# Kernel optimization log

Measured on AMD Instinct MI355X. Metric: run time of the kernel, lower is better.

Reference implementation:

```python
import jax, jax.numpy as jnp
import numpy as np

EPSILON = 1e-05
LOG_2PI = float(np.log(2.0 * np.pi))


def setup_inputs() -> dict:
    key = jax.random.key(0)
    k1, k2, k3 = jax.random.split(key, 3)
    B, S, K, N = 64, 1000, 12, 80  # batch, seq, n_states, n_channels
    x = jax.random.normal(k1, (B, S, N), dtype=jnp.float32)
    mu = jax.random.normal(k2, (B, K, N), dtype=jnp.float32)
    # Positive-definite covariances per (batch, state)
    A = jax.random.normal(k3, (B, K, N, N), dtype=jnp.float32)
    sigma = A @ jnp.swapaxes(A, -1, -2) / N + jnp.eye(N, dtype=jnp.float32)
    return {"x": x, "mu": mu, "sigma": sigma}


def reference(x, mu, sigma):
    """Batched-over-states MVN log-likelihood.

    x: (B, S, N); mu: (B, K, N); sigma: (B, K, N, N).
    Returns log_likelihood: (B, S, K).
    """
    N = x.shape[-1]
    # add_epsilon with diag=True: epsilon * I on the diagonal
    sigma = sigma + jnp.asarray(EPSILON, sigma.dtype) * jnp.eye(N, dtype=sigma.dtype)
    L = jnp.linalg.cholesky(sigma)  # (B, K, N, N), batched across states
    diff = x[:, :, None, :] - mu[:, None, :, :]  # (B, S, K, N)
    # Solve L z = diff, batched: L -> (B, 1, K, N, N), diff -> (B, S, K, N, 1)
    z = jax.scipy.linalg.solve_triangular(L[:, None], diff[..., None], lower=True)[..., 0]
    quad = jnp.sum(z * z, axis=-1)  # (B, S, K)
    logdet_half = jnp.sum(jnp.log(jnp.diagonal(L, axis1=-2, axis2=-1)), axis=-1)  # (B, K)
    ll = -0.5 * quad - logdet_half[:, None, :] - 0.5 * N * jnp.asarray(LOG_2PI, x.dtype)
    return ll  # (B, S, K)
```

## Files before the change

### kernel.cpp

```cpp
#include <hip/hip_runtime.h>

#define Bb 64
#define Ss 1000
#define Kk 12
#define Nn 80
#define CTERM 73.51508265637381f
#define STA 84

typedef __attribute__((ext_vector_type(8))) short short8;
typedef __attribute__((ext_vector_type(4))) float f32x4;

static __device__ __forceinline__ unsigned short f2bf(float f) {
    unsigned u = __builtin_bit_cast(unsigned, f);
    unsigned r = u + 0x7FFFu + ((u >> 16) & 1u);
    return (unsigned short)(r >> 16);
}
static __device__ __forceinline__ float bf2f(unsigned short h) {
    unsigned u = ((unsigned)h) << 16;
    return __builtin_bit_cast(float, u);
}

__global__ __launch_bounds__(512, 6) void prep_kernel(
    const float* __restrict__ sigma, const float* __restrict__ mu,
    const float* __restrict__ x,
    uint4* __restrict__ wsWh, uint4* __restrict__ wsWl,
    float* __restrict__ wsV, float* __restrict__ wsL,
    uint4* __restrict__ Xh, uint4* __restrict__ Xl, int doX)
{
    __shared__ float Ls[Nn * STA];
    __shared__ float invd[Nn];
    __shared__ float mus[Nn];
    __shared__ float ldp[8];
    __shared__ float vps[8 * Nn];

    const int bk  = blockIdx.x;
    const int tid = threadIdx.x;
    const int w   = tid >> 6;
    const int l   = tid & 63;
    const int r2  = l + 64;

    const float4* sp4 = (const float4*)(sigma + (size_t)bk * Nn * Nn);
    #pragma unroll
    for (int it = 0; it < 4; ++it) {
        int ci = tid + 512 * it;
        if (ci < 1600) {
            int r = ci / 20, c4 = 4 * (ci - 20 * r);
            if (c4 <= r + 3) {
                float4 v = sp4[ci];
                *(float4*)&Ls[r * STA + c4] = v;
            }
        }
    }
    if (tid < Nn) mus[tid] = mu[(size_t)bk * Nn + tid];
    __syncthreads();
    if (tid < Nn) Ls[tid * STA + tid] += 1e-5f;
    __syncthreads();

    float ldacc = 0.0f;
    for (int p = 0; p < 20; ++p) {
        const int j0 = 4 * p;
        const bool a1 = (l >= j0);
        const bool a2 = (l < 16) && (r2 >= j0);

        if (w == (p & 7)) {
            float B00 = Ls[j0*STA+j0];
            float B10 = Ls[(j0+1)*STA+j0], B11 = Ls[(j0+1)*STA+j0+1];
            float B20 = Ls[(j0+2)*STA+j0], B21 = Ls[(j0+2)*STA+j0+1], B22 = Ls[(j0+2)*STA+j0+2];
            float B30 = Ls[(j0+3)*STA+j0], B31 = Ls[(j0+3)*STA+j0+1], B32 = Ls[(j0+3)*STA+j0+2], B33 = Ls[(j0+3)*STA+j0+3];
            float rv0 = rsqrtf(B00);
            float l10 = B10*rv0, l20 = B20*rv0, l30 = B30*rv0;
            float t11 = fmaf(-l10,l10,B11);                    float rv1 = rsqrtf(t11);
            float l21 = fmaf(-l20,l10,B21)*rv1;
            float l31 = fmaf(-l30,l10,B31)*rv1;
            float t22 = fmaf(-l21,l21,fmaf(-l20,l20,B22));     float rv2 = rsqrtf(t22);
            float l32 = fmaf(-l31,l21,fmaf(-l30,l20,B32))*rv2;
            float t33 = fmaf(-l32,l32,fmaf(-l31,l31,fmaf(-l30,l30,B33)));
            float rv3 = rsqrtf(t33);
            ldacc += 0.5f * (logf(B00) + logf(t11) + logf(t22) + logf(t33));
            if (l == 0) { invd[j0]=rv0; invd[j0+1]=rv1; invd[j0+2]=rv2; invd[j0+3]=rv3; }

            if (a1) {
                float4 a = *(float4*)&Ls[l * STA + j0];
                float b0 = a.x * rv0;
                float b1 = fmaf(-l10, b0, a.y) * rv1;
                float b2 = fmaf(-l21, b1, fmaf(-l20, b0, a.z)) * rv2;
                float b3 = fmaf(-l32, b2, fmaf(-l31, b1, fmaf(-l30, b0, a.w))) * rv3;
                *(float4*)&Ls[l * STA + j0] = make_float4(b0, b1, b2, b3);
            }
            if (a2) {
                float4 a = *(float4*)&Ls[r2 * STA + j0];
                float c0 = a.x * rv0;
                float c1 = fmaf(-l10, c0, a.y) * rv1;
                float c2 = fmaf(-l21, c1, fmaf(-l20, c0, a.z)) * rv2;
                float c3 = fmaf(-l32, c2, fmaf(-l31, c1, fmaf(-l30, c0, a.w))) * rv3;
                *(float4*)&Ls[r2 * STA + j0] = make_float4(c0, c1, c2, c3);
            }
        }
        __syncthreads();

        const int gs0 = p + 1;
        const int g0 = gs0 + ((w - gs0) & 7);
        #pragma unroll 2
        for (int g = g0; g < 20; g += 8) {
            const int cb = 4 * g;
            float4 q0 = *(const float4*)&Ls[(cb+0) * STA + j0];
            float4 q1 = *(const float4*)&Ls[(cb+1) * STA + j0];
            float4 q2 = *(const float4*)&Ls[(cb+2) * STA + j0];
            float4 q3 = *(const float4*)&Ls[(cb+3) * STA + j0];
            {
                const int R = cb + l;
                if (R < Nn) {
                    float4 pv = *(const float4*)&Ls[R * STA + j0];
                    float4 t  = *(float4*)&Ls[R * STA + cb];
                    t.x = fmaf(-pv.x,q0.x, fmaf(-pv.y,q0.y, fmaf(-pv.z,q0.z, fmaf(-pv.w,q0.w, t.x))));
                    t.y = fmaf(-pv.x,q1.x, fmaf(-pv.y,q1.y, fmaf(-pv.z,q1.z, fmaf(-pv.w,q1.w, t.y))));
                    t.z = fmaf(-pv.x,q2.x, fmaf(-pv.y,q2.y, fmaf(-pv.z,q2.z, fmaf(-pv.w,q2.w, t.z))));
                    t.w = fmaf(-pv.x,q3.x, fmaf(-pv.y,q3.y, fmaf(-pv.z,q3.z, fmaf(-pv.w,q3.w, t.w))));
                    *(float4*)&Ls[R * STA + cb] = t;
                }
            }
            if (cb + 64 < Nn) {
                const int R = cb + 64 + l;
                if (R < Nn) {
                    float4 pv = *(const float4*)&Ls[R * STA + j0];
                    float4 t  = *(float4*)&Ls[R * STA + cb];
                    t.x = fmaf(-pv.x,q0.x, fmaf(-pv.y,q0.y, fmaf(-pv.z,q0.z, fmaf(-pv.w,q0.w, t.x))));
                    t.y = fmaf(-pv.x,q1.x, fmaf(-pv.y,q1.y, fmaf(-pv.z,q1.z, fmaf(-pv.w,q1.w, t.y))));
                    t.z = fmaf(-pv.x,q2.x, fmaf(-pv.y,q2.y, fmaf(-pv.z,q2.z, fmaf(-pv.w,q2.w, t.z))));
                    t.w = fmaf(-pv.x,q3.x, fmaf(-pv.y,q3.y, fmaf(-pv.z,q3.z, fmaf(-pv.w,q3.w, t.w))));
                    *(float4*)&Ls[R * STA + cb] = t;
                }
            }
        }
    }
    if (l == 0) ldp[w] = ldacc;
    __syncthreads();
    if (tid == 0) wsL[bk] = ldp[0]+ldp[1]+ldp[2]+ldp[3]+ldp[4]+ldp[5]+ldp[6]+ldp[7];

    for (int i = tid; i < Nn * Nn; i += 512) {
        int r = i / Nn, c = i - Nn * r;
        if (c > r) Ls[r * STA + c] = 0.0f;
    }
    __syncthreads();

    for (int p = 0; p < 20; ++p) {
        const int i0 = 4 * p;
        const bool b1a = (i0 + 3 >= l);
        const bool b2a = (l < 16) && (i0 + 3 >= r2);

        if (w == (p & 7)) {
            float m10 = Ls[(i0+1)*STA + i0];
            float m20 = Ls[(i0+2)*STA + i0];
            float m30 = Ls[(i0+3)*STA + i0];
            float m21 = Ls[(i0+2)*STA + i0+1];
            float m31 = Ls[(i0+3)*STA + i0+1];
            float m32 = Ls[(i0+3)*STA + i0+2];
            float4 iv = *(const float4*)&invd[i0];
            if (b1a) {
                float4 a = *(float4*)&Ls[l * STA + i0];
                if (l >= i0)
                    a = make_float4(l==i0?1.f:0.f, l==i0+1?1.f:0.f, l==i0+2?1.f:0.f, l==i0+3?1.f:0.f);
                float w0 = a.x * iv.x;
                float w1 = fmaf(-w0, m10, a.y) * iv.y;
                float w2 = fmaf(-w1, m21, fmaf(-w0, m20, a.z)) * iv.z;
                float w3 = fmaf(-w2, m32, fmaf(-w1, m31, fmaf(-w0, m30, a.w))) * iv.w;
                *(float4*)&Ls[l * STA + i0] = make_float4(w0, w1, w2, w3);
            }
            if (b2a) {
                float4 a = *(float4*)&Ls[r2 * STA + i0];
                if (r2 >= i0)
                    a = make_float4(r2==i0?1.f:0.f, r2==i0+1?1.f:0.f, r2==i0+2?1.f:0.f, r2==i0+3?1.f:0.f);
                float v0 = a.x * iv.x;
                float v1 = fmaf(-v0, m10, a.y) * iv.y;
                float v2 = fmaf(-v1, m21, fmaf(-v0, m20, a.z)) * iv.z;
                float v3 = fmaf(-v2, m32, fmaf(-v1, m31, fmaf(-v0, m30, a.w))) * iv.w;
                *(float4*)&Ls[r2 * STA + i0] = make_float4(v0, v1, v2, v3);
            }
        }
        __syncthreads();

        float4 wv = make_float4(0.f,0.f,0.f,0.f), vv = make_float4(0.f,0.f,0.f,0.f);
        if (b1a) wv = *(float4*)&Ls[l * STA + i0];
        if (b2a) vv = *(float4*)&Ls[r2 * STA + i0];
        if (b1a | b2a) {
            const int gs0 = p + 1;
            const int g0 = gs0 + ((w - gs0) & 7);
            for (int g = g0; g < 20; g += 8) {
                float4 q0 = *(const float4*)&Ls[(4*g+0) * STA + i0];
                float4 q1 = *(const float4*)&Ls[(4*g+1) * STA + i0];
                float4 q2 = *(const float4*)&Ls[(4*g+2) * STA + i0];
                float4 q3 = *(const float4*)&Ls[(4*g+3) * STA + i0];
                if (b1a) {
                    float4 t = *(float4*)&Ls[l * STA + 4*g];
                    t.x = fmaf(-wv.x,q0.x, fmaf(-wv.y,q0.y, fmaf(-wv.z,q0.z, fmaf(-wv.w,q0.w, t.x))));
                    t.y = fmaf(-wv.x,q1.x, fmaf(-wv.y,q1.y, fmaf(-wv.z,q1.z, fmaf(-wv.w,q1.w, t.y))));
                    t.z = fmaf(-wv.x,q2.x, fmaf(-wv.y,q2.y, fmaf(-wv.z,q2.z, fmaf(-wv.w,q2.w, t.z))));
                    t.w = fmaf(-wv.x,q3.x, fmaf(-wv.y,q3.y, fmaf(-wv.z,q3.z, fmaf(-wv.w,q3.w, t.w))));
                    *(float4*)&Ls[l * STA + 4*g] = t;
                }
                if (b2a) {
                    float4 t = *(float4*)&Ls[r2 * STA + 4*g];
                    t.x = fmaf(-vv.x,q0.x, fmaf(-vv.y,q0.y, fmaf(-vv.z,q0.z, fmaf(-vv.w,q0.w, t.x))));
                    t.y = fmaf(-vv.x,q1.x, fmaf(-vv.y,q1.y, fmaf(-vv.z,q1.z, fmaf(-vv.w,q1.w, t.y))));
                    t.z = fmaf(-vv.x,q2.x, fmaf(-vv.y,q2.y, fmaf(-vv.z,q2.z, fmaf(-vv.w,q2.w, t.z))));
                    t.w = fmaf(-vv.x,q3.x, fmaf(-vv.y,q3.y, fmaf(-vv.z,q3.z, fmaf(-vv.w,q3.w, t.w))));
                    *(float4*)&Ls[r2 * STA + 4*g] = t;
                }
            }
        }
    }
    __syncthreads();

    {
        float s1 = 0.f, s2 = 0.f;
        const int c0 = 10 * w;
        #pragma unroll 2
        for (int cc = 0; cc < 10; ++cc) {
            int c = c0 + cc;
            float mc = mus[c];
            float e1 = (c <= l)  ? Ls[c * STA + l]  : 0.f;
            s1 = fmaf(e1, mc, s1);
            if (l < 16) {
                float e2 = (c <= r2) ? Ls[c * STA + r2] : 0.f;
                s2 = fmaf(e2, mc, s2);
            }
        }
        vps[w * Nn + l] = s1;
        if (l < 16) vps[w * Nn + r2] = s2;
        __syncthreads();
        if (tid < Nn) {
            float acc = 0.f;
            #pragma unroll
            for (int ww = 0; ww < 8; ++ww) acc += vps[ww * Nn + tid];
            wsV[(size_t)bk * Nn + tid] = acc;
        }
    }

    const int n = l & 15, quad = l >> 4;
    uint4* ph = wsWh + (size_t)bk * 800;
    uint4* pq = wsWl + (size_t)bk * 800;
    for (int f = w; f < 10; f += 8) {
        int ks = f / 5, mt = f - 5 * ks;
        int m = 16 * mt + n, kb = 32 * ks + 8 * quad;
        unsigned hh[8], lo[8];
        #pragma unroll
        for (int j = 0; j < 8; ++j) {
            float wj = (m >= kb + j) ? Ls[(kb + j) * STA + m] : 0.f;
            unsigned short h = f2bf(wj);
            hh[j] = h; lo[j] = f2bf(wj - bf2f(h));
        }
        ph[f*64 + l] = make_uint4(hh[0]|(hh[1]<<16), hh[2]|(hh[3]<<16), hh[4]|(hh[5]<<16), hh[6]|(hh[7]<<16));
        pq[f*64 + l] = make_uint4(lo[0]|(lo[1]<<16), lo[2]|(lo[3]<<16), lo[4]|(lo[5]<<16), lo[6]|(lo[7]<<16));
    }
    if (w < 5) {
        int mt = w;
        if (quad < 2) {
            int m = 16 * mt + n, kb = 64 + 8 * quad;
            unsigned hh[8], lo[8];
            #pragma unroll
            for (int j = 0; j < 8; ++j) {
                float wj = (m >= kb + j) ? Ls[(kb + j) * STA + m] : 0.f;
                unsigned short h = f2bf(wj);
                hh[j] = h; lo[j] = f2bf(wj - bf2f(h));
            }
            ph[640 + mt*32 + l] = make_uint4(hh[0]|(hh[1]<<16), hh[2]|(hh[3]<<16), hh[4]|(hh[5]<<16), hh[6]|(hh[7]<<16));
            pq[640 + mt*32 + l] = make_uint4(lo[0]|(lo[1]<<16), lo[2]|(lo[3]<<16), lo[4]|(lo[5]<<16), lo[6]|(lo[7]<<16));
        }
    }

    if (doX) {
        const int wid = bk * 8 + w;
        const int qd = l >> 4, n2 = l & 15;
        #pragma unroll
        for (int it = 0; it < 2; ++it) {
            int G = wid + 6144 * it;
            if (G >= 12096) break;
            int b2  = G / 189;
            int rem = G - b2 * 189;
            int sg  = rem / 3, ks = rem - 3 * sg;
            int s   = sg * 16 + n2;
            int k0  = 32 * ks + 8 * qd;
            float d[8] = {0.f,0.f,0.f,0.f,0.f,0.f,0.f,0.f};
            if (s < Ss) {
                const float* xp = x + ((size_t)b2 * Ss + s) * Nn + k0;
                float4 f0 = *(const float4*)xp;
                float4 f1 = *(const float4*)(xp + 4);
                d[0]=f0.x; d[1]=f0.y; d[2]=f0.z; d[3]=f0.w;
                d[4]=f1.x; d[5]=f1.y; d[6]=f1.z; d[7]=f1.w;
            }
            unsigned hh[8], lo[8];
            #pragma unroll
            for (int j = 0; j < 8; ++j) {
                unsigned short h = f2bf(d[j]);
                hh[j] = h; lo[j] = f2bf(d[j] - bf2f(h));
            }
            size_t slot = ((size_t)(b2 * 64 + sg) * 3 + ks) * 64 + l;
            Xh[slot] = make_uint4(hh[0]|(hh[1]<<16), hh[2]|(hh[3]<<16), hh[4]|(hh[5]<<16), hh[6]|(hh[7]<<16));
            Xl[slot] = make_uint4(lo[0]|(lo[1]<<16), lo[2]|(lo[3]<<16), lo[4]|(lo[5]<<16), lo[6]|(lo[7]<<16));
        }
    }
}

__global__ __launch_bounds__(256) void ll_kernel2(
    const uint4* __restrict__ Xh, const uint4* __restrict__ Xl,
    const uint4* __restrict__ wsWh, const uint4* __restrict__ wsWl,
    const float* __restrict__ wsV, const float* __restrict__ wsL,
    float* __restrict__ out)
{
    __shared__ uint4 WhL[960], WlL[960];
    const int b = blockIdx.x;
    const int k = blockIdx.y;
    const int bk = b * Kk + k;
    const int tid = threadIdx.x;
    const int wv = tid >> 6, lane = tid & 63;
    const int n = lane & 15, quad = lane >> 4;

    const uint4* gh = wsWh + (size_t)bk * 800;
    const uint4* gl = wsWl + (size_t)bk * 800;
    #pragma unroll
    for (int it = 0; it < 3; ++it) {
        int i = tid + 256 * it;
        if (i < 640) { WhL[i] = gh[i]; WlL[i] = gl[i]; }
    }
    #pragma unroll
    for (int it = 0; it < 2; ++it) {
        int i = tid + 256 * it;
        if (i < 320) {
            int mt = i >> 6, ln = i & 63, qd = (ln >> 4);
            uint4 vh = make_uint4(0,0,0,0), vl = make_uint4(0,0,0,0);
            if (qd < 2) { vh = gh[640 + mt*32 + ln]; vl = gl[640 + mt*32 + ln]; }
            WhL[640 + i] = vh; WlL[640 + i] = vl;
        }
    }
    __syncthreads();

    const float ld = wsL[bk];
    f32x4 vf[5];
    #pragma unroll
    for (int mt = 0; mt < 5; ++mt)
        vf[mt] = *(const f32x4*)&wsV[(size_t)bk * Nn + 16*mt + 4*quad];

    for (int st = 0; st < 8; ++st) {
        const int sg0 = st * 8 + wv * 2;
        short8 bh[2][3], bl[2][3];
        #pragma unroll
        for (int t = 0; t < 2; ++t)
            #pragma unroll
            for (int ks = 0; ks < 3; ++ks) {
                size_t base = ((size_t)(b * 64 + sg0 + t) * 3 + ks) * 64 + lane;
                bh[t][ks] = __builtin_bit_cast(short8, Xh[base]);
                bl[t][ks] = __builtin_bit_cast(short8, Xl[base]);
            }

        f32x4 acc[2][5];
        #pragma unroll
        for (int t = 0; t < 2; ++t)
            #pragma unroll
            for (int mt = 0; mt < 5; ++mt) acc[t][mt] = (f32x4){0.f,0.f,0.f,0.f};

        #pragma unroll
        for (int ks = 0; ks < 3; ++ks) {
            #pragma unroll
            for (int mt = 0; mt < 5; ++mt) {
                const int fi = (ks < 2) ? (ks*5 + mt)*64 + lane : 640 + mt*64 + lane;
                short8 wh = __builtin_bit_cast(short8, WhL[fi]);
                short8 wl = __builtin_bit_cast(short8, WlL[fi]);
                #pragma unroll
                for (int t = 0; t < 2; ++t) {
                    acc[t][mt] = __builtin_amdgcn_mfma_f32_16x16x32_bf16(wh, bh[t][ks], acc[t][mt], 0, 0, 0);
                    acc[t][mt] = __builtin_amdgcn_mfma_f32_16x16x32_bf16(wl, bh[t][ks], acc[t][mt], 0, 0, 0);
                    acc[t][mt] = __builtin_amdgcn_mfma_f32_16x16x32_bf16(wh, bl[t][ks], acc[t][mt], 0, 0, 0);
                }
            }
        }

        #pragma unroll
        for (int t = 0; t < 2; ++t) {
            float q2 = 0.f;
            #pragma unroll
            for (int mt = 0; mt < 5; ++mt)
                #pragma unroll
                for (int r = 0; r < 4; ++r) {
                    float y = acc[t][mt][r] - vf[mt][r];
                    q2 = fmaf(y, y, q2);
                }
            q2 += __shfl_xor(q2, 16, 64);
            q2 += __shfl_xor(q2, 32, 64);
            int gs = st * 128 + wv * 32 + 16 * t + n;
            if (lane < 16 && gs < Ss)
                out[((size_t)b * Ss + gs) * Kk + k] = -0.5f * q2 - ld - CTERM;
        }
    }
}

__global__ __launch_bounds__(256) void ll_kernel(
    const float* __restrict__ x,
    const uint4* __restrict__ wsWh, const uint4* __restrict__ wsWl,
    const float* __restrict__ wsV, const float* __restrict__ wsL,
    float* __restrict__ out)
{
    const int b    = blockIdx.x;
    const int st   = blockIdx.y;
    const int tid  = threadIdx.x;
    const int wv   = tid >> 6, lane = tid & 63;
    const int n    = lane & 15, quad = lane >> 4;
    const int sbase = st * 128 + wv * 32;

    short8 xh[2][3], xl[2][3];
    #pragma unroll
    for (int t = 0; t < 2; ++t) {
        int gs = sbase + 16 * t + n;
        #pragma unroll
        for (int ks = 0; ks < 3; ++ks) {
            int kb = 32 * ks + 8 * quad;
            float d[8] = {0.f,0.f,0.f,0.f,0.f,0.f,0.f,0.f};
            if (gs < Ss && kb < Nn) {
                const float* xp = x + ((size_t)b * Ss + gs) * Nn + kb;
                float4 f0 = *(const float4*)xp;
                float4 f1 = *(const float4*)(xp + 4);
                d[0]=f0.x; d[1]=f0.y; d[2]=f0.z; d[3]=f0.w;
                d[4]=f1.x; d[5]=f1.y; d[6]=f1.z; d[7]=f1.w;
            }
            short8 h, lo2;
            #pragma unroll
            for (int j = 0; j < 8; ++j) {
                unsigned short hv = f2bf(d[j]);
                h[j]   = (short)hv;
                lo2[j] = (short)f2bf(d[j] - bf2f(hv));
            }
            xh[t][ks] = h; xl[t][ks] = lo2;
        }
    }

    for (int k = 0; k < Kk; ++k) {
        const int bk = b * Kk + k;
        const uint4* ah_p = wsWh + (size_t)bk * 800;
        const uint4* al_p = wsWl + (size_t)bk * 800;

        f32x4 acc[2][5];
        #pragma unroll
        for (int t = 0; t < 2; ++t)
            #pragma unroll
            for (int mt = 0; mt < 5; ++mt) acc[t][mt] = (f32x4){0.f,0.f,0.f,0.f};

        #pragma unroll
        for (int ks = 0; ks < 3; ++ks) {
            short8 ah[5], al[5];
            if (ks < 2) {
                #pragma unroll
                for (int mt = 0; mt < 5; ++mt) {
                    ah[mt] = __builtin_bit_cast(short8, ah_p[(ks*5 + mt)*64 + lane]);
                    al[mt] = __builtin_bit_cast(short8, al_p[(ks*5 + mt)*64 + lane]);
                }
            } else {
                #pragma unroll
                for (int mt = 0; mt < 5; ++mt) {
                    uint4 zh = make_uint4(0,0,0,0), zl = make_uint4(0,0,0,0);
                    if (quad < 2) {
                        zh = ah_p[640 + mt*32 + lane];
                        zl = al_p[640 + mt*32 + lane];
                    }
                    ah[mt] = __builtin_bit_cast(short8, zh);
                    al[mt] = __builtin_bit_cast(short8, zl);
                }
            }
            #pragma unroll
            for (int mt = 0; mt < 5; ++mt)
                #pragma unroll
                for (int t = 0; t < 2; ++t) {
                    acc[t][mt] = __builtin_amdgcn_mfma_f32_16x16x32_bf16(ah[mt], xh[t][ks], acc[t][mt], 0, 0, 0);
                    acc[t][mt] = __builtin_amdgcn_mfma_f32_16x16x32_bf16(al[mt], xh[t][ks], acc[t][mt], 0, 0, 0);
                    acc[t][mt] = __builtin_amdgcn_mfma_f32_16x16x32_bf16(ah[mt], xl[t][ks], acc[t][mt], 0, 0, 0);
                }
        }

        float ld = wsL[bk];
        f32x4 vf[5];
        #pragma unroll
        for (int mt = 0; mt < 5; ++mt)
            vf[mt] = *(const f32x4*)&wsV[(size_t)bk * Nn + 16*mt + 4*quad];
        #pragma unroll
        for (int t = 0; t < 2; ++t) {
            float q2 = 0.f;
            #pragma unroll
            for (int mt = 0; mt < 5; ++mt)
                #pragma unroll
                for (int r = 0; r < 4; ++r) {
                    float y = acc[t][mt][r] - vf[mt][r];
                    q2 = fmaf(y, y, q2);
                }
            q2 += __shfl_xor(q2, 16, 64);
            q2 += __shfl_xor(q2, 32, 64);
            int gs = sbase + 16 * t + n;
            if (lane < 16 && gs < Ss)
                out[((size_t)b * Ss + gs) * Kk + k] = -0.5f * q2 - ld - CTERM;
        }
    }
}

#define ST1 81
__global__ __launch_bounds__(256) void mvn_ll_fallback(
    const float* __restrict__ x, const float* __restrict__ mu,
    const float* __restrict__ sigma, float* __restrict__ out)
{
    __shared__ float Ls[Nn * ST1];
    __shared__ float invd[Nn];
    __shared__ float mus[Nn];
    __shared__ float logdet_s;

    const int bk = blockIdx.x, b = bk / Kk, k = bk - b * Kk;
    const int tid = threadIdx.x, nt = blockDim.x;

    const float* sp = sigma + (size_t)bk * Nn * Nn;
    for (int t = tid; t < Nn * Nn; t += nt) Ls[(t / Nn) * ST1 + (t % Nn)] = sp[t];
    if (tid < Nn) mus[tid] = mu[(size_t)bk * Nn + tid];
    __syncthreads();
    if (tid < Nn) Ls[tid * ST1 + tid] += 1e-5f;
    __syncthreads();
    for (int j = 0; j < Nn; ++j) {
        if (tid == 0) {
            float d = sqrtf(Ls[j * ST1 + j]);
            Ls[j * ST1 + j] = d; invd[j] = 1.0f / d;
        }
        __syncthreads();
        const float inv = invd[j];
        for (int i = j + 1 + tid; i < Nn; i += nt) Ls[i * ST1 + j] *= inv;
        __syncthreads();
        for (int t = tid; t < Nn * Nn; t += nt) {
            int r = t / Nn, c = t % Nn;
            if (r > j && c > j && c <= r)
                Ls[r * ST1 + c] -= Ls[r * ST1 + j] * Ls[c * ST1 + j];
        }
        __syncthreads();
    }
    if (tid == 0) {
        float a = 0.f; for (int j = 0; j < Nn; ++j) a += logf(Ls[j * ST1 + j]);
        logdet_s = a;
    }
    __syncthreads();
    const float ld = logdet_s;
    for (int s = tid; s < Ss; s += nt) {
        const float4* xp = (const float4*)(x + ((size_t)b * Ss + s) * Nn);
        float a[Nn];
        #pragma unroll
        for (int q = 0; q < Nn / 4; ++q) {
            float4 v = xp[q];
            a[4*q+0] = v.x - mus[4*q+0]; a[4*q+1] = v.y - mus[4*q+1];
            a[4*q+2] = v.z - mus[4*q+2]; a[4*q+3] = v.w - mus[4*q+3];
        }
        #pragma unroll
        for (int i = 0; i < Nn; ++i) {
            float t = a[i];
            #pragma unroll
            for (int j = 0; j < i; ++j) t = fmaf(-Ls[i * ST1 + j], a[j], t);
            a[i] = t * invd[i];
        }
        float quad = 0.f;
        #pragma unroll
        for (int i = 0; i < Nn; ++i) quad = fmaf(a[i], a[i], quad);
        out[((size_t)b * Ss + s) * Kk + k] = -0.5f * quad - ld - CTERM;
    }
}

extern "C" void kernel_launch(void* const* d_in, const int* in_sizes, int n_in,
                              void* d_out, int out_size, void* d_ws, size_t ws_size,
                              hipStream_t stream) {
    const float* x     = (const float*)d_in[0];
    const float* mu    = (const float*)d_in[1];
    const float* sigma = (const float*)d_in[2];
    float* out = (float*)d_out;

    const size_t nBK   = (size_t)Bb * Kk;
    const size_t nWu4  = nBK * 800;
    const size_t nXu4  = (size_t)Bb * 64 * 3 * 64;
    const size_t need_mid  = nWu4 * 16 * 2 + nBK * Nn * 4 + nBK * 4;
    const size_t need_full = need_mid + nXu4 * 16 * 2;

    if (ws_size >= need_full) {
        uint4* wsWh = (uint4*)d_ws;
        uint4* wsWl = wsWh + nWu4;
        uint4* Xh   = wsWl + nWu4;
        uint4* Xl   = Xh + nXu4;
        float* wsV  = (float*)(Xl + nXu4);
        float* wsL  = wsV + nBK * Nn;
        prep_kernel<<<dim3(Bb * Kk), dim3(512), 0, stream>>>(
            sigma, mu, x, wsWh, wsWl, wsV, wsL, Xh, Xl, 1);
        ll_kernel2<<<dim3(Bb, Kk), dim3(256), 0, stream>>>(Xh, Xl, wsWh, wsWl, wsV, wsL, out);
    } else if (ws_size >= need_mid) {
        uint4* wsWh = (uint4*)d_ws;
        uint4* wsWl = wsWh + nWu4;
        float* wsV  = (float*)(wsWl + nWu4);
        float* wsL  = wsV + nBK * Nn;
        prep_kernel<<<dim3(Bb * Kk), dim3(512), 0, stream>>>(
            sigma, mu, x, wsWh, wsWl, wsV, wsL, (uint4*)nullptr, (uint4*)nullptr, 0);
        ll_kernel<<<dim3(Bb, 8), dim3(256), 0, stream>>>(x, wsWh, wsWl, wsV, wsL, out);
    } else {
        mvn_ll_fallback<<<dim3(Bb * Kk), dim3(256), 0, stream>>>(x, mu, sigma, out);
    }
}
```

Before: 161.6 us.

## Run Cholesky and inverse in a single wave, overlapping X conversion on second wave

The prep kernel shrinks from 512 to 128 threads. Wave 0 now does the whole Cholesky factorisation, triangular inverse and mu projection alone, with no block barriers. Wave 1 meanwhile converts x into split-bf16 tiles, and both waves then pack the W fragments. This removes roughly 40 __syncthreads per block and the shared-memory reductions, and also switches to fast __logf. The cost is serialising the factorisation into one wave, so per-block latency grows while more blocks can be resident per CU.

Result: slower. 209.5 us (+29.6%).

```diff
diff --git a/kernel.cpp b/kernel.cpp
--- a/kernel.cpp
+++ b/kernel.cpp
@@ -20,7 +20,7 @@
     return __builtin_bit_cast(float, u);
 }
 
-__global__ __launch_bounds__(512, 6) void prep_kernel(
+__global__ __launch_bounds__(128, 2) void prep_kernel(
     const float* __restrict__ sigma, const float* __restrict__ mu,
     const float* __restrict__ x,
     uint4* __restrict__ wsWh, uint4* __restrict__ wsWl,
@@ -30,8 +30,6 @@
     __shared__ float Ls[Nn * STA];
     __shared__ float invd[Nn];
     __shared__ float mus[Nn];
-    __shared__ float ldp[8];
-    __shared__ float vps[8 * Nn];
 
     const int bk  = blockIdx.x;
     const int tid = threadIdx.x;
@@ -39,30 +37,23 @@
     const int l   = tid & 63;
     const int r2  = l + 64;
 
-    const float4* sp4 = (const float4*)(sigma + (size_t)bk * Nn * Nn);
-    #pragma unroll
-    for (int it = 0; it < 4; ++it) {
-        int ci = tid + 512 * it;
-        if (ci < 1600) {
+    if (w == 0) {
+        const float4* sp4 = (const float4*)(sigma + (size_t)bk * Nn * Nn);
+        #pragma unroll
+        for (int it = 0; it < 25; ++it) {
+            int ci = l + 64 * it;
             int r = ci / 20, c4 = 4 * (ci - 20 * r);
-            if (c4 <= r + 3) {
-                float4 v = sp4[ci];
-                *(float4*)&Ls[r * STA + c4] = v;
-            }
-        }
-    }
-    if (tid < Nn) mus[tid] = mu[(size_t)bk * Nn + tid];
-    __syncthreads();
-    if (tid < Nn) Ls[tid * STA + tid] += 1e-5f;
-    __syncthreads();
-
-    float ldacc = 0.0f;
-    for (int p = 0; p < 20; ++p) {
-        const int j0 = 4 * p;
-        const bool a1 = (l >= j0);
-        const bool a2 = (l < 16) && (r2 >= j0);
-
-        if (w == (p & 7)) {
+            if (c4 <= r + 3)
+                *(float4*)&Ls[r * STA + c4] = sp4[ci];
+        }
+        mus[l] = mu[(size_t)bk * Nn + l];
+        if (l < 16) mus[r2] = mu[(size_t)bk * Nn + r2];
+        Ls[l * STA + l] += 1e-5f;
+        if (l < 16) Ls[r2 * STA + r2] += 1e-5f;
+
+        float ldacc = 0.0f;
+        for (int p = 0; p < 20; ++p) {
+            const int j0 = 4 * p;
             float B00 = Ls[j0*STA+j0];
             float B10 = Ls[(j0+1)*STA+j0], B11 = Ls[(j0+1)*STA+j0+1];
             float B20 = Ls[(j0+2)*STA+j0], B21 = Ls[(j0+2)*STA+j0+1], B22 = Ls[(j0+2)*STA+j0+2];
@@ -76,10 +67,10 @@
             float l32 = fmaf(-l31,l21,fmaf(-l30,l20,B32))*rv2;
             float t33 = fmaf(-l32,l32,fmaf(-l31,l31,fmaf(-l30,l30,B33)));
             float rv3 = rsqrtf(t33);
-            ldacc += 0.5f * (logf(B00) + logf(t11) + logf(t22) + logf(t33));
+            ldacc += 0.5f * (__logf(B00) + __logf(t11) + __logf(t22) + __logf(t33));
             if (l == 0) { invd[j0]=rv0; invd[j0+1]=rv1; invd[j0+2]=rv2; invd[j0+3]=rv3; }
 
-            if (a1) {
+            if (l >= j0) {
                 float4 a = *(float4*)&Ls[l * STA + j0];
                 float b0 = a.x * rv0;
                 float b1 = fmaf(-l10, b0, a.y) * rv1;
@@ -87,7 +78,7 @@
                 float b3 = fmaf(-l32, b2, fmaf(-l31, b1, fmaf(-l30, b0, a.w))) * rv3;
                 *(float4*)&Ls[l * STA + j0] = make_float4(b0, b1, b2, b3);
             }
-            if (a2) {
+            if (l < 16 && r2 >= j0) {
                 float4 a = *(float4*)&Ls[r2 * STA + j0];
                 float c0 = a.x * rv0;
                 float c1 = fmaf(-l10, c0, a.y) * rv1;
@@ -95,60 +86,47 @@
                 float c3 = fmaf(-l32, c2, fmaf(-l31, c1, fmaf(-l30, c0, a.w))) * rv3;
                 *(float4*)&Ls[r2 * STA + j0] = make_float4(c0, c1, c2, c3);
             }
-        }
-        __syncthreads();
-
-        const int gs0 = p + 1;
-        const int g0 = gs0 + ((w - gs0) & 7);
-        #pragma unroll 2
-        for (int g = g0; g < 20; g += 8) {
-            const int cb = 4 * g;
-            float4 q0 = *(const float4*)&Ls[(cb+0) * STA + j0];
-            float4 q1 = *(const float4*)&Ls[(cb+1) * STA + j0];
-            float4 q2 = *(const float4*)&Ls[(cb+2) * STA + j0];
-            float4 q3 = *(const float4*)&Ls[(cb+3) * STA + j0];
-            {
-                const int R = cb + l;
-                if (R < Nn) {
-                    float4 pv = *(const float4*)&Ls[R * STA + j0];
-                    float4 t  = *(float4*)&Ls[R * STA + cb];
-                    t.x = fmaf(-pv.x,q0.x, fmaf(-pv.y,q0.y, fmaf(-pv.z,q0.z, fmaf(-pv.w,q0.w, t.x))));
-                    t.y = fmaf(-pv.x,q1.x, fmaf(-pv.y,q1.y, fmaf(-pv.z,q1.z, fmaf(-pv.w,q1.w, t.y))));
-                    t.z = fmaf(-pv.x,q2.x, fmaf(-pv.y,q2.y, fmaf(-pv.z,q2.z, fmaf(-pv.w,q2.w, t.z))));
-                    t.w = fmaf(-pv.x,q3.x, fmaf(-pv.y,q3.y, fmaf(-pv.z,q3.z, fmaf(-pv.w,q3.w, t.w))));
-                    *(float4*)&Ls[R * STA + cb] = t;
-                }
-            }
-            if (cb + 64 < Nn) {
-                const int R = cb + 64 + l;
-                if (R < Nn) {
-                    float4 pv = *(const float4*)&Ls[R * STA + j0];
-                    float4 t  = *(float4*)&Ls[R * STA + cb];
-                    t.x = fmaf(-pv.x,q0.x, fmaf(-pv.y,q0.y, fmaf(-pv.z,q0.z, fmaf(-pv.w,q0.w, t.x))));
-                    t.y = fmaf(-pv.x,q1.x, fmaf(-pv.y,q1.y, fmaf(-pv.z,q1.z, fmaf(-pv.w,q1.w, t.y))));
-                    t.z = fmaf(-pv.x,q2.x, fmaf(-pv.y,q2.y, fmaf(-pv.z,q2.z, fmaf(-pv.w,q2.w, t.z))));
-                    t.w = fmaf(-pv.x,q3.x, fmaf(-pv.y,q3.y, fmaf(-pv.z,q3.z, fmaf(-pv.w,q3.w, t.w))));
-                    *(float4*)&Ls[R * STA + cb] = t;
-                }
-            }
-        }
-    }
-    if (l == 0) ldp[w] = ldacc;
-    __syncthreads();
-    if (tid == 0) wsL[bk] = ldp[0]+ldp[1]+ldp[2]+ldp[3]+ldp[4]+ldp[5]+ldp[6]+ldp[7];
-
-    for (int i = tid; i < Nn * Nn; i += 512) {
-        int r = i / Nn, c = i - Nn * r;
-        if (c > r) Ls[r * STA + c] = 0.0f;
-    }
-    __syncthreads();
-
-    for (int p = 0; p < 20; ++p) {
-        const int i0 = 4 * p;
-        const bool b1a = (i0 + 3 >= l);
-        const bool b2a = (l < 16) && (i0 + 3 >= r2);
-
-        if (w == (p & 7)) {
+
+            #pragma unroll 2
+            for (int g = p + 1; g < 20; ++g) {
+                const int cb = 4 * g;
+                float4 q0 = *(const float4*)&Ls[(cb+0) * STA + j0];
+                float4 q1 = *(const float4*)&Ls[(cb+1) * STA + j0];
+                float4 q2 = *(const float4*)&Ls[(cb+2) * STA + j0];
+                float4 q3 = *(const float4*)&Ls[(cb+3) * STA + j0];
+                {
+                    const int R = cb + l;
+                    if (R < Nn) {
+                        float4 pv = *(const float4*)&Ls[R * STA + j0];
+                        float4 t  = *(float4*)&Ls[R * STA + cb];
+                        t.x = fmaf(-pv.x,q0.x, fmaf(-pv.y,q0.y, fmaf(-pv.z,q0.z, fmaf(-pv.w,q0.w, t.x))));
+                        t.y = fmaf(-pv.x,q1.x, fmaf(-pv.y,q1.y, fmaf(-pv.z,q1.z, fmaf(-pv.w,q1.w, t.y))));
+                        t.z = fmaf(-pv.x,q2.x, fmaf(-pv.y,q2.y, fmaf(-pv.z,q2.z, fmaf(-pv.w,q2.w, t.z))));
+                        t.w = fmaf(-pv.x,q3.x, fmaf(-pv.y,q3.y, fmaf(-pv.z,q3.z, fmaf(-pv.w,q3.w, t.w))));
+                        *(float4*)&Ls[R * STA + cb] = t;
+                    }
+                }
+                if (cb + 64 < Nn) {
+                    const int R = cb + 64 + l;
+                    if (R < Nn) {
+                        float4 pv = *(const float4*)&Ls[R * STA + j0];
+                        float4 t  = *(float4*)&Ls[R * STA + cb];
+                        t.x = fmaf(-pv.x,q0.x, fmaf(-pv.y,q0.y, fmaf(-pv.z,q0.z, fmaf(-pv.w,q0.w, t.x))));
+                        t.y = fmaf(-pv.x,q1.x, fmaf(-pv.y,q1.y, fmaf(-pv.z,q1.z, fmaf(-pv.w,q1.w, t.y))));
+                        t.z = fmaf(-pv.x,q2.x, fmaf(-pv.y,q2.y, fmaf(-pv.z,q2.z, fmaf(-pv.w,q2.w, t.z))));
+                        t.w = fmaf(-pv.x,q3.x, fmaf(-pv.y,q3.y, fmaf(-pv.z,q3.z, fmaf(-pv.w,q3.w, t.w))));
+                        *(float4*)&Ls[R * STA + cb] = t;
+                    }
+                }
+            }
+        }
+        if (l == 0) wsL[bk] = ldacc;
+
+        for (int p = 0; p < 20; ++p) {
+            const int i0 = 4 * p;
+            const bool b1a = (i0 + 3 >= l);
+            const bool b2a = (l < 16) && (i0 + 3 >= r2);
+
             float m10 = Ls[(i0+1)*STA + i0];
             float m20 = Ls[(i0+2)*STA + i0];
             float m30 = Ls[(i0+3)*STA + i0];
@@ -156,124 +134,85 @@
             float m31 = Ls[(i0+3)*STA + i0+1];
             float m32 = Ls[(i0+3)*STA + i0+2];
             float4 iv = *(const float4*)&invd[i0];
+
+            float sw0=0.f, sw1=0.f, sw2=0.f, sw3=0.f;
+            float sv0=0.f, sv1=0.f, sv2=0.f, sv3=0.f;
             if (b1a) {
-                float4 a = *(float4*)&Ls[l * STA + i0];
+                float4 a;
                 if (l >= i0)
                     a = make_float4(l==i0?1.f:0.f, l==i0+1?1.f:0.f, l==i0+2?1.f:0.f, l==i0+3?1.f:0.f);
-                float w0 = a.x * iv.x;
-                float w1 = fmaf(-w0, m10, a.y) * iv.y;
-                float w2 = fmaf(-w1, m21, fmaf(-w0, m20, a.z)) * iv.z;
-                float w3 = fmaf(-w2, m32, fmaf(-w1, m31, fmaf(-w0, m30, a.w))) * iv.w;
-                *(float4*)&Ls[l * STA + i0] = make_float4(w0, w1, w2, w3);
+                else
+                    a = *(float4*)&Ls[l * STA + i0];
+                sw0 = a.x * iv.x;
+                sw1 = fmaf(-sw0, m10, a.y) * iv.y;
+                sw2 = fmaf(-sw1, m21, fmaf(-sw0, m20, a.z)) * iv.z;
+                sw3 = fmaf(-sw2, m32, fmaf(-sw1, m31, fmaf(-sw0, m30, a.w))) * iv.w;
+                *(float4*)&Ls[l * STA + i0] = make_float4(sw0, sw1, sw2, sw3);
             }
             if (b2a) {
-                float4 a = *(float4*)&Ls[r2 * STA + i0];
+                float4 a;
                 if (r2 >= i0)
                     a = make_float4(r2==i0?1.f:0.f, r2==i0+1?1.f:0.f, r2==i0+2?1.f:0.f, r2==i0+3?1.f:0.f);
-                float v0 = a.x * iv.x;
-                float v1 = fmaf(-v0, m10, a.y) * iv.y;
-                float v2 = fmaf(-v1, m21, fmaf(-v0, m20, a.z)) * iv.z;
-                float v3 = fmaf(-v2, m32, fmaf(-v1, m31, fmaf(-v0, m30, a.w))) * iv.w;
-                *(float4*)&Ls[r2 * STA + i0] = make_float4(v0, v1, v2, v3);
-            }
-        }
-        __syncthreads();
-
-        float4 wv = make_float4(0.f,0.f,0.f,0.f), vv = make_float4(0.f,0.f,0.f,0.f);
-        if (b1a) wv = *(float4*)&Ls[l * STA + i0];
-        if (b2a) vv = *(float4*)&Ls[r2 * STA + i0];
-        if (b1a | b2a) {
-            const int gs0 = p + 1;
-            const int g0 = gs0 + ((w - gs0) & 7);
-            for (int g = g0; g < 20; g += 8) {
-                float4 q0 = *(const float4*)&Ls[(4*g+0) * STA + i0];
-                float4 q1 = *(const float4*)&Ls[(4*g+1) * STA + i0];
-                float4 q2 = *(const float4*)&Ls[(4*g+2) * STA + i0];
-                float4 q3 = *(const float4*)&Ls[(4*g+3) * STA + i0];
-                if (b1a) {
-                    float4 t = *(float4*)&Ls[l * STA + 4*g];
-                    t.x = fmaf(-wv.x,q0.x, fmaf(-wv.y,q0.y, fmaf(-wv.z,q0.z, fmaf(-wv.w,q0.w, t.x))));
-                    t.y = fmaf(-wv.x,q1.x, fmaf(-wv.y,q1.y, fmaf(-wv.z,q1.z, fmaf(-wv.w,q1.w, t.y))));
-                    t.z = fmaf(-wv.x,q2.x, fmaf(-wv.y,q2.y, fmaf(-wv.z,q2.z, fmaf(-wv.w,q2.w, t.z))));
-                    t.w = fmaf(-wv.x,q3.x, fmaf(-wv.y,q3.y, fmaf(-wv.z,q3.z, fmaf(-wv.w,q3.w, t.w))));
-                    *(float4*)&Ls[l * STA + 4*g] = t;
-                }
-                if (b2a) {
-                    float4 t = *(float4*)&Ls[r2 * STA + 4*g];
-                    t.x = fmaf(-vv.x,q0.x, fmaf(-vv.y,q0.y, fmaf(-vv.z,q0.z, fmaf(-vv.w,q0.w, t.x))));
-                    t.y = fmaf(-vv.x,q1.x, fmaf(-vv.y,q1.y, fmaf(-vv.z,q1.z, fmaf(-vv.w,q1.w, t.y))));
-                    t.z = fmaf(-vv.x,q2.x, fmaf(-vv.y,q2.y, fmaf(-vv.z,q2.z, fmaf(-vv.w,q2.w, t.z))));
-                    t.w = fmaf(-vv.x,q3.x, fmaf(-vv.y,q3.y, fmaf(-vv.z,q3.z, fmaf(-vv.w,q3.w, t.w))));
-                    *(float4*)&Ls[r2 * STA + 4*g] = t;
-                }
-            }
-        }
-    }
-    __syncthreads();
-
-    {
-        float s1 = 0.f, s2 = 0.f;
-        const int c0 = 10 * w;
-        #pragma unroll 2
-        for (int cc = 0; cc < 10; ++cc) {
-            int c = c0 + cc;
-            float mc = mus[c];
-            float e1 = (c <= l)  ? Ls[c * STA + l]  : 0.f;
-            s1 = fmaf(e1, mc, s1);
-            if (l < 16) {
-                float e2 = (c <= r2) ? Ls[c * STA + r2] : 0.f;
-                s2 = fmaf(e2, mc, s2);
-            }
-        }
-        vps[w * Nn + l] = s1;
-        if (l < 16) vps[w * Nn + r2] = s2;
-        __syncthreads();
-        if (tid < Nn) {
-            float acc = 0.f;
-            #pragma unroll
-            for (int ww = 0; ww < 8; ++ww) acc += vps[ww * Nn + tid];
-            wsV[(size_t)bk * Nn + tid] = acc;
-        }
-    }
-
-    const int n = l & 15, quad = l >> 4;
-    uint4* ph = wsWh + (size_t)bk * 800;
-    uint4* pq = wsWl + (size_t)bk * 800;
-    for (int f = w; f < 10; f += 8) {
-        int ks = f / 5, mt = f - 5 * ks;
-        int m = 16 * mt + n, kb = 32 * ks + 8 * quad;
-        unsigned hh[8], lo[8];
-        #pragma unroll
-        for (int j = 0; j < 8; ++j) {
-            float wj = (m >= kb + j) ? Ls[(kb + j) * STA + m] : 0.f;
-            unsigned short h = f2bf(wj);
-            hh[j] = h; lo[j] = f2bf(wj - bf2f(h));
-        }
-        ph[f*64 + l] = make_uint4(hh[0]|(hh[1]<<16), hh[2]|(hh[3]<<16), hh[4]|(hh[5]<<16), hh[6]|(hh[7]<<16));
-        pq[f*64 + l] = make_uint4(lo[0]|(lo[1]<<16), lo[2]|(lo[3]<<16), lo[4]|(lo[5]<<16), lo[6]|(lo[7]<<16));
-    }
-    if (w < 5) {
-        int mt = w;
-        if (quad < 2) {
-            int m = 16 * mt + n, kb = 64 + 8 * quad;
-            unsigned hh[8], lo[8];
-            #pragma unroll
-            for (int j = 0; j < 8; ++j) {
-                float wj = (m >= kb + j) ? Ls[(kb + j) * STA + m] : 0.f;
-                unsigned short h = f2bf(wj);
-                hh[j] = h; lo[j] = f2bf(wj - bf2f(h));
-            }
-            ph[640 + mt*32 + l] = make_uint4(hh[0]|(hh[1]<<16), hh[2]|(hh[3]<<16), hh[4]|(hh[5]<<16), hh[6]|(hh[7]<<16));
-            pq[640 + mt*32 + l] = make_uint4(lo[0]|(lo[1]<<16), lo[2]|(lo[3]<<16), lo[4]|(lo[5]<<16), lo[6]|(lo[7]<<16));
-        }
-    }
-
-    if (doX) {
-        const int wid = bk * 8 + w;
+                else
+                    a = *(float4*)&Ls[r2 * STA + i0];
+                sv0 = a.x * iv.x;
+                sv1 = fmaf(-sv0, m10, a.y) * iv.y;
+                sv2 = fmaf(-sv1, m21, fmaf(-sv0, m20, a.z)) * iv.z;
+                sv3 = fmaf(-sv2, m32, fmaf(-sv1, m31, fmaf(-sv0, m30, a.w))) * iv.w;
+                *(float4*)&Ls[r2 * STA + i0] = make_float4(sv0, sv1, sv2, sv3);
+            }
+
+            if (b1a | b2a) {
+                #pragma unroll 2
+                for (int g = p + 1; g < 20; ++g) {
+                    const int cb = 4 * g;
+                    float4 q0 = *(const float4*)&Ls[(cb+0) * STA + i0];
+                    float4 q1 = *(const float4*)&Ls[(cb+1) * STA + i0];
+                    float4 q2 = *(const float4*)&Ls[(cb+2) * STA + i0];
+                    float4 q3 = *(const float4*)&Ls[(cb+3) * STA + i0];
+                    if (b1a) {
+                        float4 t;
+                        if (l >= i0) t = make_float4(0.f, 0.f, 0.f, 0.f);
+                        else         t = *(float4*)&Ls[l * STA + cb];
+                        t.x = fmaf(-sw0,q0.x, fmaf(-sw1,q0.y, fmaf(-sw2,q0.z, fmaf(-sw3,q0.w, t.x))));
+                        t.y = fmaf(-sw0,q1.x, fmaf(-sw1,q1.y, fmaf(-sw2,q1.z, fmaf(-sw3,q1.w, t.y))));
+                        t.z = fmaf(-sw0,q2.x, fmaf(-sw1,q2.y, fmaf(-sw2,q2.z, fmaf(-sw3,q2.w, t.z))));
+                        t.w = fmaf(-sw0,q3.x, fmaf(-sw1,q3.y, fmaf(-sw2,q3.z, fmaf(-sw3,q3.w, t.w))));
+                        *(float4*)&Ls[l * STA + cb] = t;
+                    }
+                    if (b2a) {
+                        float4 t;
+                        if (r2 >= i0) t = make_float4(0.f, 0.f, 0.f, 0.f);
+                        else          t = *(float4*)&Ls[r2 * STA + cb];
+                        t.x = fmaf(-sv0,q0.x, fmaf(-sv1,q0.y, fmaf(-sv2,q0.z, fmaf(-sv3,q0.w, t.x))));
+                        t.y = fmaf(-sv0,q1.x, fmaf(-sv1,q1.y, fmaf(-sv2,q1.z, fmaf(-sv3,q1.w, t.y))));
+                        t.z = fmaf(-sv0,q2.x, fmaf(-sv1,q2.y, fmaf(-sv2,q2.z, fmaf(-sv3,q2.w, t.z))));
+                        t.w = fmaf(-sv0,q3.x, fmaf(-sv1,q3.y, fmaf(-sv2,q3.z, fmaf(-sv3,q3.w, t.w))));
+                        *(float4*)&Ls[r2 * STA + cb] = t;
+                    }
+                }
+            }
+        }
+
+        {
+            float s1 = 0.f, s2 = 0.f;
+            #pragma unroll 4
+            for (int c = 0; c < Nn; ++c) {
+                float mc = mus[c];
+                float e1 = (c <= l)  ? Ls[c * STA + l]  : 0.f;
+                s1 = fmaf(e1, mc, s1);
+                if (l < 16) {
+                    float e2 = (c <= r2) ? Ls[c * STA + r2] : 0.f;
+                    s2 = fmaf(e2, mc, s2);
+                }
+            }
+            wsV[(size_t)bk * Nn + l] = s1;
+            if (l < 16) wsV[(size_t)bk * Nn + r2] = s2;
+        }
+    } else if (doX) {
         const int qd = l >> 4, n2 = l & 15;
-        #pragma unroll
-        for (int it = 0; it < 2; ++it) {
-            int G = wid + 6144 * it;
+        for (int it = 0; it < 16; ++it) {
+            int G = bk + 768 * it;
             if (G >= 12096) break;
             int b2  = G / 189;
             int rem = G - b2 * 189;
@@ -299,6 +238,38 @@
             Xl[slot] = make_uint4(lo[0]|(lo[1]<<16), lo[2]|(lo[3]<<16), lo[4]|(lo[5]<<16), lo[6]|(lo[7]<<16));
         }
     }
+    __syncthreads();
+
+    const int n = l & 15, quad = l >> 4;
+    uint4* ph = wsWh + (size_t)bk * 800;
+    uint4* pq = wsWl + (size_t)bk * 800;
+    for (int f = w; f < 10; f += 2) {
+        int ks = f / 5, mt = f - 5 * ks;
+        int m = 16 * mt + n, kb = 32 * ks + 8 * quad;
+        unsigned hh[8], lo[8];
+        #pragma unroll
+        for (int j = 0; j < 8; ++j) {
+            float wj = (m >= kb + j) ? Ls[(kb + j) * STA + m] : 0.f;
+            unsigned short h = f2bf(wj);
+            hh[j] = h; lo[j] = f2bf(wj - bf2f(h));
+        }
+        ph[f*64 + l] = make_uint4(hh[0]|(hh[1]<<16), hh[2]|(hh[3]<<16), hh[4]|(hh[5]<<16), hh[6]|(hh[7]<<16));
+        pq[f*64 + l] = make_uint4(lo[0]|(lo[1]<<16), lo[2]|(lo[3]<<16), lo[4]|(lo[5]<<16), lo[6]|(lo[7]<<16));
+    }
+    for (int mt = w; mt < 5; mt += 2) {
+        if (quad < 2) {
+            int m = 16 * mt + n, kb = 64 + 8 * quad;
+            unsigned hh[8], lo[8];
+            #pragma unroll
+            for (int j = 0; j < 8; ++j) {
+                float wj = (m >= kb + j) ? Ls[(kb + j) * STA + m] : 0.f;
+                unsigned short h = f2bf(wj);
+                hh[j] = h; lo[j] = f2bf(wj - bf2f(h));
+            }
+            ph[640 + mt*32 + l] = make_uint4(hh[0]|(hh[1]<<16), hh[2]|(hh[3]<<16), hh[4]|(hh[5]<<16), hh[6]|(hh[7]<<16));
+            pq[640 + mt*32 + l] = make_uint4(lo[0]|(lo[1]<<16), lo[2]|(lo[3]<<16), lo[4]|(lo[5]<<16), lo[6]|(lo[7]<<16));
+        }
+    }
 }
 
 __global__ __launch_bounds__(256) void ll_kernel2(
@@ -583,7 +554,7 @@
         uint4* Xl   = Xh + nXu4;
         float* wsV  = (float*)(Xl + nXu4);
         float* wsL  = wsV + nBK * Nn;
-        prep_kernel<<<dim3(Bb * Kk), dim3(512), 0, stream>>>(
+        prep_kernel<<<dim3(Bb * Kk), dim3(128), 0, stream>>>(
             sigma, mu, x, wsWh, wsWl, wsV, wsL, Xh, Xl, 1);
         ll_kernel2<<<dim3(Bb, Kk), dim3(256), 0, stream>>>(Xh, Xl, wsWh, wsWl, wsV, wsL, out);
     } else if (ws_size >= need_mid) {
@@ -591,7 +562,7 @@
         uint4* wsWl = wsWh + nWu4;
         float* wsV  = (float*)(wsWl + nWu4);
         float* wsL  = wsV + nBK * Nn;
-        prep_kernel<<<dim3(Bb * Kk), dim3(512), 0, stream>>>(
+        prep_kernel<<<dim3(Bb * Kk), dim3(128), 0, stream>>>(
             sigma, mu, x, wsWh, wsWl, wsV, wsL, (uint4*)nullptr, (uint4*)nullptr, 0);
         ll_kernel<<<dim3(Bb, 8), dim3(256), 0, stream>>>(x, wsWh, wsWl, wsV, wsL, out);
     } else {
```
